# Optimization experiments

Hardware: AMD Instinct MI355X
Metric: run time of the kernel (lower is better)

## Reference

```python
import jax, jax.numpy as jnp
import numpy as np

D_MODEL = 4096
NUM_EXPERTS = 64


def setup_inputs() -> dict:
    key = jax.random.key(0)
    kx, kw, kb = jax.random.split(key, 3)
    x = jax.random.normal(kx, (4, 4096, D_MODEL), dtype=jnp.float32)
    # nn.Linear(d_model, num_experts): weight [E, D], bias [E]
    bound = 1.0 / np.sqrt(D_MODEL)
    W = jax.random.uniform(kw, (NUM_EXPERTS, D_MODEL), dtype=jnp.float32, minval=-bound, maxval=bound)
    b = jax.random.uniform(kb, (NUM_EXPERTS,), dtype=jnp.float32, minval=-bound, maxval=bound)
    return {"x": x, "W": W, "b": b}


def reference(x, W, b):
    # logits: [B, S, E]
    logits = jnp.einsum('bsd,ed->bse', x, W) + b
    scores = jax.nn.softmax(logits, axis=-1)
    val, idx = jax.lax.top_k(scores, 2)            # [B, S, 2]
    # scatter top-2 values back into a dense [B, S, E] dispatch mask
    onehot = jax.nn.one_hot(idx, NUM_EXPERTS, dtype=scores.dtype)  # [B, S, 2, E]
    dispatch = jnp.einsum('bsk,bske->bse', val, onehot)
    combine = dispatch
    expert_counts = dispatch.sum(axis=(0, 1))      # [E]
    return dispatch, combine, expert_counts
```

## Files before the change

kernel.cpp:

```cpp
#include <hip/hip_runtime.h>
#include <math.h>

#define D_MODEL 4096
#define NEXP    64
#define NTOK    16384
#define NSL     4
#define NCH     4
#define KS      256
#define BMT     128

typedef __attribute__((ext_vector_type(8))) short  bf16x8;
typedef __attribute__((ext_vector_type(4))) float  f32x4;

__device__ __forceinline__ unsigned short f2bf_rn(float f) {
    union { float f; unsigned u; } v; v.f = f;
    unsigned r = v.u + 0x7fffu + ((v.u >> 16) & 1u);
    return (unsigned short)(r >> 16);
}
__device__ __forceinline__ float bf2f(unsigned short h) {
    union { unsigned u; float f; } v; v.u = ((unsigned)h) << 16;
    return v.f;
}
__device__ __forceinline__ void split2(float f0, float f1, unsigned& hw, unsigned& lw) {
    unsigned short h0 = f2bf_rn(f0), h1 = f2bf_rn(f1);
    unsigned short l0 = f2bf_rn(f0 - bf2f(h0)), l1 = f2bf_rn(f1 - bf2f(h1));
    hw = (unsigned)h0 | ((unsigned)h1 << 16);
    lw = (unsigned)l0 | ((unsigned)l1 << 16);
}
__device__ __forceinline__ void gload16(f32x4& r, const float* p) {
    asm volatile("global_load_dwordx4 %0, %1, off" : "=v"(r) : "v"(p));
}

#define WAITV_(n) asm volatile("s_waitcnt vmcnt(" #n ")" ::: "memory")
#define WAITV(n)  WAITV_(n)

__global__ __launch_bounds__(256)
void k0_prep(const float* __restrict__ W, unsigned short* __restrict__ ws,
             float* __restrict__ logits, float* __restrict__ out) {
    const int gid = blockIdx.x * 256 + threadIdx.x;
    if (blockIdx.x == 0 && threadIdx.x < NEXP)
        out[(size_t)2 * NTOK * NEXP + threadIdx.x] = 0.f;
    float4 z = make_float4(0.f, 0.f, 0.f, 0.f);
    float* lz = logits + (size_t)gid * 16;
#pragma unroll
    for (int k = 0; k < 4; ++k)
        *reinterpret_cast<float4*>(&lz[k * 4]) = z;
    int i = gid * 4;
    float4 v = *reinterpret_cast<const float4*>(&W[i]);
    unsigned short h[4], l[4];
    float f[4] = {v.x, v.y, v.z, v.w};
#pragma unroll
    for (int k = 0; k < 4; ++k) {
        h[k] = f2bf_rn(f[k]);
        l[k] = f2bf_rn(f[k] - bf2f(h[k]));
    }
    *reinterpret_cast<short4*>(&ws[i])                  = make_short4(h[0], h[1], h[2], h[3]);
    *reinterpret_cast<short4*>(&ws[NEXP * D_MODEL + i]) = make_short4(l[0], l[1], l[2], l[3]);
}

__global__ __launch_bounds__(512, 4)
void k1_gemm(const float* __restrict__ x, const unsigned short* __restrict__ wsplit,
             float* __restrict__ logits) {
    __shared__ uint4 whi[NEXP * 32];
    __shared__ uint4 wlo[NEXP * 32];

    const int tid = threadIdx.x;
    const int t0  = (blockIdx.x >> 2) * BMT;
    const int sp  = blockIdx.x & 3;

    const int lane = tid & 63;
    const int rowl = lane & 15;
    const int grp  = lane >> 4;
    const int wtok = t0 + (tid >> 6) * 16;

    f32x4 acc[4];
#pragma unroll
    for (int n = 0; n < 4; ++n)
        acc[n] = (f32x4){0.f, 0.f, 0.f, 0.f};

#define STEPX(kb, WN, c0, c1, DOI) do {                                      \
    WAITV(WN);                                                               \
    __builtin_amdgcn_sched_barrier(0);                                       \
    union { bf16x8 v; unsigned u[4]; } ah, al;                               \
    split2(c0.x, c0.y, ah.u[0], al.u[0]);                                    \
    split2(c0.z, c0.w, ah.u[1], al.u[1]);                                    \
    split2(c1.x, c1.y, ah.u[2], al.u[2]);                                    \
    split2(c1.z, c1.w, ah.u[3], al.u[3]);                                    \
    if (DOI) {                                                               \
        gload16(c0, xp0 + ((kb) + 2) * 32);                                  \
        gload16(c1, xp0 + ((kb) + 2) * 32 + 4);                              \
    }                                                                        \
    const int c  = (kb) * 4 + grp;                                           \
    const int cs = (c & 24) | ((c & 7) ^ (rowl & 7));     \
    _Pragma("unroll")                                                        \
    for (int n = 0; n < 4; ++n) {                                            \
        const int idx = (n * 16 + rowl) * 32 + cs;                           \
        bf16x8 bh = *reinterpret_cast<const bf16x8*>(&whi[idx]);             \
        bf16x8 bl = *reinterpret_cast<const bf16x8*>(&wlo[idx]);             \
        acc[n] = __builtin_amdgcn_mfma_f32_16x16x32_bf16(ah.v, bh, acc[n], 0, 0, 0); \
        acc[n] = __builtin_amdgcn_mfma_f32_16x16x32_bf16(ah.v, bl, acc[n], 0, 0, 0); \
        acc[n] = __builtin_amdgcn_mfma_f32_16x16x32_bf16(al.v, bh, acc[n], 0, 0, 0); \
    }                                                                        \
} while (0)

    for (int half = 0; half < NCH; ++half) {
        const int ks0 = (sp * NCH + half) * KS;
        if (half) __syncthreads();

#pragma unroll
        for (int i = 0; i < 4; ++i) {
            int p  = tid + i * 512;
            int e  = p >> 5;
            int c  = p & 31;
            int cs = (c & 24) | ((c & 7) ^ (e & 7));
            const unsigned short* src = wsplit + (size_t)e * D_MODEL + ks0 + c * 8;
            whi[e * 32 + cs] = *reinterpret_cast<const uint4*>(src);
            wlo[e * 32 + cs] = *reinterpret_cast<const uint4*>(src + NEXP * D_MODEL);
        }
        __syncthreads();

        const float* xp0 = x + (size_t)(wtok + rowl) * D_MODEL + ks0 + grp * 8;

        f32x4 xA0, xA1, xB0, xB1;
        gload16(xA0, xp0);      gload16(xA1, xp0 + 4);
        gload16(xB0, xp0 + 32); gload16(xB1, xp0 + 36);

        STEPX(0, 2, xA0, xA1, 1);
        STEPX(1, 2, xB0, xB1, 1);
        STEPX(2, 2, xA0, xA1, 1);
        STEPX(3, 2, xB0, xB1, 1);
        STEPX(4, 2, xA0, xA1, 1);
        STEPX(5, 2, xB0, xB1, 1);
        STEPX(6, 2, xA0, xA1, 0);
        STEPX(7, 0, xB0, xB1, 0);
    }

#pragma unroll
    for (int n = 0; n < 4; ++n)
#pragma unroll
        for (int i = 0; i < 4; ++i) {
            const int t = wtok + grp * 4 + i;
            const int e = n * 16 + rowl;
            atomicAdd(&logits[(size_t)t * NEXP + e], acc[n][i]);
        }
}

__global__ __launch_bounds__(128)
void k2_softmax_top2(const float* __restrict__ logits, const float* __restrict__ bias,
                     float* __restrict__ out) {
    const int t = blockIdx.x * 128 + threadIdx.x;
    __shared__ float cnt[NEXP];
    __shared__ float bs[NEXP];
    if (threadIdx.x < NEXP) {
        cnt[threadIdx.x] = 0.f;
        bs[threadIdx.x]  = bias[threadIdx.x];
    }
    __syncthreads();

    float l[NEXP];
    const float* lp = logits + (size_t)t * NEXP;
#pragma unroll
    for (int g = 0; g < 16; ++g) {
        float4 v = *reinterpret_cast<const float4*>(&lp[g * 4]);
        l[4 * g + 0] = v.x + bs[4 * g + 0];
        l[4 * g + 1] = v.y + bs[4 * g + 1];
        l[4 * g + 2] = v.z + bs[4 * g + 2];
        l[4 * g + 3] = v.w + bs[4 * g + 3];
    }

    float m = l[0];
#pragma unroll
    for (int e = 1; e < NEXP; ++e) m = fmaxf(m, l[e]);

    float sum = 0.f;
#pragma unroll
    for (int e = 0; e < NEXP; ++e) sum += __expf(l[e] - m);

    float v1 = -INFINITY, v2 = -INFINITY;
    int   i1 = 0, i2 = 0;
#pragma unroll
    for (int e = 0; e < NEXP; ++e) {
        if (l[e] > v1) { v2 = v1; i2 = i1; v1 = l[e]; i1 = e; }
        else if (l[e] > v2) { v2 = l[e]; i2 = e; }
    }
    const float inv = 1.f / sum;
    const float s1 = __expf(v1 - m) * inv;
    const float s2 = __expf(v2 - m) * inv;

    float* disp = out + (size_t)t * NEXP;
    float* comb = out + (size_t)NTOK * NEXP + (size_t)t * NEXP;
#pragma unroll
    for (int g = 0; g < 16; ++g) {
        float4 o = make_float4(0.f, 0.f, 0.f, 0.f);
        if ((i1 >> 2) == g) (&o.x)[i1 & 3] = s1;
        if ((i2 >> 2) == g) (&o.x)[i2 & 3] = s2;
        *reinterpret_cast<float4*>(&disp[g * 4]) = o;
        *reinterpret_cast<float4*>(&comb[g * 4]) = o;
    }

    atomicAdd(&cnt[i1], s1);
    atomicAdd(&cnt[i2], s2);
    __syncthreads();
    if (threadIdx.x < NEXP)
        atomicAdd(&out[(size_t)2 * NTOK * NEXP + threadIdx.x], cnt[threadIdx.x]);
}

extern "C" void kernel_launch(void* const* d_in, const int* in_sizes, int n_in,
                              void* d_out, int out_size, void* d_ws, size_t ws_size,
                              hipStream_t stream) {
    const float* x = (const float*)d_in[0];
    const float* W = (const float*)d_in[1];
    const float* b = (const float*)d_in[2];
    float* out = (float*)d_out;
    unsigned short* ws = (unsigned short*)d_ws;
    float* logits = (float*)(ws + 2 * NEXP * D_MODEL);

    k0_prep<<<256, 256, 0, stream>>>(W, ws, logits, out);
    k1_gemm<<<(NTOK / BMT) * NSL, 512, 0, stream>>>(x, ws, logits);
    k2_softmax_top2<<<NTOK / 128, 128, 0, stream>>>(logits, b, out);
}
```

Baseline: 84.43 us.

## Double-buffer split weight chunks in LDS with register prefetch

The GEMM kernel now splits K into eight 128-wide chunks instead of four 256-wide ones and keeps two LDS buffers for the hi/lo bf16 weights. The next chunk's weights are loaded into registers while MFMAs run on the current buffer, then written to the other buffer, so each chunk needs one barrier instead of two. The aim is to hide weight-staging latency and barrier stalls behind compute. The cost is a shorter x-load pipeline per chunk with more prologue/drain bubbles. The weight prefetch loads also share the in-order vmcnt counter with the x loads, which may force early waits on them.

Result: faster. 82.63 us (median of 2 runs) (-2.1%).

```diff
diff --git a/kernel.cpp b/kernel.cpp
--- a/kernel.cpp
+++ b/kernel.cpp
@@ -5,8 +5,8 @@
 #define NEXP    64
 #define NTOK    16384
 #define NSL     4
-#define NCH     4
-#define KS      256
+#define NCH     8
+#define KS      128
 #define BMT     128
 
 typedef __attribute__((ext_vector_type(8))) short  bf16x8;
@@ -61,8 +61,8 @@
 __global__ __launch_bounds__(512, 4)
 void k1_gemm(const float* __restrict__ x, const unsigned short* __restrict__ wsplit,
              float* __restrict__ logits) {
-    __shared__ uint4 whi[NEXP * 32];
-    __shared__ uint4 wlo[NEXP * 32];
+    __shared__ uint4 whi[2][NEXP * 16];
+    __shared__ uint4 wlo[2][NEXP * 16];
 
     const int tid = threadIdx.x;
     const int t0  = (blockIdx.x >> 2) * BMT;
@@ -73,66 +73,87 @@
     const int grp  = lane >> 4;
     const int wtok = t0 + (tid >> 6) * 16;
 
+    const int e0 = tid >> 4,          c0 = tid & 15;
+    const int e1 = (tid + 512) >> 4,  c1 = tid & 15;
+    const int cs0 = (c0 & 8) | ((c0 & 7) ^ (e0 & 7));
+    const int cs1 = (c1 & 8) | ((c1 & 7) ^ (e1 & 7));
+
     f32x4 acc[4];
 #pragma unroll
     for (int n = 0; n < 4; ++n)
         acc[n] = (f32x4){0.f, 0.f, 0.f, 0.f};
 
-#define STEPX(kb, WN, c0, c1, DOI) do {                                      \
+    {
+        const int ks00 = sp * (NCH * KS);
+        const unsigned short* s0 = wsplit + (size_t)e0 * D_MODEL + ks00 + c0 * 8;
+        const unsigned short* s1 = wsplit + (size_t)e1 * D_MODEL + ks00 + c1 * 8;
+        whi[0][e0 * 16 + cs0] = *reinterpret_cast<const uint4*>(s0);
+        wlo[0][e0 * 16 + cs0] = *reinterpret_cast<const uint4*>(s0 + NEXP * D_MODEL);
+        whi[0][e1 * 16 + cs1] = *reinterpret_cast<const uint4*>(s1);
+        wlo[0][e1 * 16 + cs1] = *reinterpret_cast<const uint4*>(s1 + NEXP * D_MODEL);
+    }
+    __syncthreads();
+
+#define STEPX(kb, WN, c0r, c1r, DOI, BH, BL) do {                            \
     WAITV(WN);                                                               \
     __builtin_amdgcn_sched_barrier(0);                                       \
     union { bf16x8 v; unsigned u[4]; } ah, al;                               \
-    split2(c0.x, c0.y, ah.u[0], al.u[0]);                                    \
-    split2(c0.z, c0.w, ah.u[1], al.u[1]);                                    \
-    split2(c1.x, c1.y, ah.u[2], al.u[2]);                                    \
-    split2(c1.z, c1.w, ah.u[3], al.u[3]);                                    \
+    split2(c0r.x, c0r.y, ah.u[0], al.u[0]);                                  \
+    split2(c0r.z, c0r.w, ah.u[1], al.u[1]);                                  \
+    split2(c1r.x, c1r.y, ah.u[2], al.u[2]);                                  \
+    split2(c1r.z, c1r.w, ah.u[3], al.u[3]);                                  \
     if (DOI) {                                                               \
-        gload16(c0, xp0 + ((kb) + 2) * 32);                                  \
-        gload16(c1, xp0 + ((kb) + 2) * 32 + 4);                              \
+        gload16(c0r, xp0 + ((kb) + 2) * 32);                                 \
+        gload16(c1r, xp0 + ((kb) + 2) * 32 + 4);                             \
     }                                                                        \
     const int c  = (kb) * 4 + grp;                                           \
-    const int cs = (c & 24) | ((c & 7) ^ (rowl & 7));     \
+    const int cs = (c & 8) | ((c & 7) ^ (rowl & 7));      \
     _Pragma("unroll")                                                        \
     for (int n = 0; n < 4; ++n) {                                            \
-        const int idx = (n * 16 + rowl) * 32 + cs;                           \
-        bf16x8 bh = *reinterpret_cast<const bf16x8*>(&whi[idx]);             \
-        bf16x8 bl = *reinterpret_cast<const bf16x8*>(&wlo[idx]);             \
+        const int idx = (n * 16 + rowl) * 16 + cs;                           \
+        bf16x8 bh = *reinterpret_cast<const bf16x8*>(&BH[idx]);              \
+        bf16x8 bl = *reinterpret_cast<const bf16x8*>(&BL[idx]);              \
         acc[n] = __builtin_amdgcn_mfma_f32_16x16x32_bf16(ah.v, bh, acc[n], 0, 0, 0); \
         acc[n] = __builtin_amdgcn_mfma_f32_16x16x32_bf16(ah.v, bl, acc[n], 0, 0, 0); \
         acc[n] = __builtin_amdgcn_mfma_f32_16x16x32_bf16(al.v, bh, acc[n], 0, 0, 0); \
     }                                                                        \
 } while (0)
 
-    for (int half = 0; half < NCH; ++half) {
-        const int ks0 = (sp * NCH + half) * KS;
-        if (half) __syncthreads();
-
-#pragma unroll
-        for (int i = 0; i < 4; ++i) {
-            int p  = tid + i * 512;
-            int e  = p >> 5;
-            int c  = p & 31;
-            int cs = (c & 24) | ((c & 7) ^ (e & 7));
-            const unsigned short* src = wsplit + (size_t)e * D_MODEL + ks0 + c * 8;
-            whi[e * 32 + cs] = *reinterpret_cast<const uint4*>(src);
-            wlo[e * 32 + cs] = *reinterpret_cast<const uint4*>(src + NEXP * D_MODEL);
+#pragma unroll
+    for (int ch = 0; ch < NCH; ++ch) {
+        const int ks0 = sp * (NCH * KS) + ch * KS;
+
+        uint4 wh0, wl0, wh1, wl1;
+        if (ch + 1 < NCH) {
+            const unsigned short* s0 = wsplit + (size_t)e0 * D_MODEL + ks0 + KS + c0 * 8;
+            const unsigned short* s1 = wsplit + (size_t)e1 * D_MODEL + ks0 + KS + c1 * 8;
+            wh0 = *reinterpret_cast<const uint4*>(s0);
+            wl0 = *reinterpret_cast<const uint4*>(s0 + NEXP * D_MODEL);
+            wh1 = *reinterpret_cast<const uint4*>(s1);
+            wl1 = *reinterpret_cast<const uint4*>(s1 + NEXP * D_MODEL);
         }
-        __syncthreads();
-
+        __builtin_amdgcn_sched_barrier(0);
+
+        const uint4* BH = &whi[ch & 1][0];
+        const uint4* BL = &wlo[ch & 1][0];
         const float* xp0 = x + (size_t)(wtok + rowl) * D_MODEL + ks0 + grp * 8;
 
         f32x4 xA0, xA1, xB0, xB1;
         gload16(xA0, xp0);      gload16(xA1, xp0 + 4);
         gload16(xB0, xp0 + 32); gload16(xB1, xp0 + 36);
 
-        STEPX(0, 2, xA0, xA1, 1);
-        STEPX(1, 2, xB0, xB1, 1);
-        STEPX(2, 2, xA0, xA1, 1);
-        STEPX(3, 2, xB0, xB1, 1);
-        STEPX(4, 2, xA0, xA1, 1);
-        STEPX(5, 2, xB0, xB1, 1);
-        STEPX(6, 2, xA0, xA1, 0);
-        STEPX(7, 0, xB0, xB1, 0);
+        STEPX(0, 2, xA0, xA1, 1, BH, BL);
+        STEPX(1, 2, xB0, xB1, 1, BH, BL);
+        STEPX(2, 2, xA0, xA1, 0, BH, BL);
+        STEPX(3, 0, xB0, xB1, 0, BH, BL);
+
+        if (ch + 1 < NCH) {
+            whi[(ch + 1) & 1][e0 * 16 + cs0] = wh0;
+            wlo[(ch + 1) & 1][e0 * 16 + cs0] = wl0;
+            whi[(ch + 1) & 1][e1 * 16 + cs1] = wh1;
+            wlo[(ch + 1) & 1][e1 * 16 + cs1] = wl1;
+            __syncthreads();
+        }
     }
 
 #pragma unroll
```
